# Optimization experiments

Measured on AMD Instinct MI355X. Metric: run time of the kernel, lower is better.

## Reference

```python
import jax, jax.numpy as jnp
import numpy as np

C = 32          # d_model / channels
D_STATE = 32
D_CONV = 4
EXPAND = 2
D_INNER = EXPAND * C          # 64
DT_RANK = (C + 15) // 16      # ceil(32/16) = 2
EPS = 1e-5


def _conv2d(x, w, b):
    # x: (B,C,H,W), w: (O,I,3,3), stride 1, padding 1 (torch Conv2d)
    y = jax.lax.conv_general_dilated(
        x, w, window_strides=(1, 1), padding=[(1, 1), (1, 1)],
        dimension_numbers=("NCHW", "OIHW", "NCHW"))
    return y + b[None, :, None, None]


def _silu(x):
    return x * jax.nn.sigmoid(x)


def _mamba(xs, in_proj_w, conv1d_w, conv1d_b, x_proj_w, dt_proj_w, dt_proj_b,
           A_log, Dp, out_proj_w):
    # xs: (B, L, C)
    xz = xs @ in_proj_w.T                       # (B, L, 2*D_INNER)
    xm, z = jnp.split(xz, 2, axis=-1)           # each (B, L, D_INNER)

    # causal depthwise conv1d along L (torch: padding=d_conv-1 then [..., :L])
    xc = xm.transpose(0, 2, 1)                  # (B, D_INNER, L)
    xc = jax.lax.conv_general_dilated(
        xc, conv1d_w, window_strides=(1,), padding=[(D_CONV - 1, 0)],
        dimension_numbers=("NCH", "OIH", "NCH"),
        feature_group_count=D_INNER)
    xm = _silu((xc + conv1d_b[None, :, None]).transpose(0, 2, 1))  # (B,L,D_INNER)

    x_dbl = xm @ x_proj_w.T                     # (B, L, DT_RANK + 2*D_STATE)
    dt = x_dbl[..., :DT_RANK]
    Bm = x_dbl[..., DT_RANK:DT_RANK + D_STATE]  # (B, L, N)
    Cm = x_dbl[..., DT_RANK + D_STATE:]         # (B, L, N)

    delta = jax.nn.softplus(dt @ dt_proj_w.T + dt_proj_b)  # (B, L, D_INNER)
    A = -jnp.exp(A_log)                                     # (D_INNER, N)

    deltaA = jnp.exp(delta[..., None] * A)                           # (B,L,D,N)
    deltaBx = delta[..., None] * Bm[:, :, None, :] * xm[..., None]   # (B,L,D,N)

    def combine(c1, c2):
        a1, b1 = c1
        a2, b2 = c2
        return a1 * a2, a2 * b1 + b2

    # parallel linear recurrence h_t = deltaA_t * h_{t-1} + deltaBx_t
    _, hstate = jax.lax.associative_scan(combine, (deltaA, deltaBx), axis=1)

    y = jnp.einsum("bldn,bln->bld", hstate, Cm) + xm * Dp
    y = y * _silu(z)
    return y @ out_proj_w.T                     # (B, L, C)


def setup_inputs() -> dict:
    key = jax.random.key(0)
    ks = jax.random.split(key, 16)
    s = 0.02
    inp = {
        "x": jax.random.normal(ks[0], (4, C, 64, 64), dtype=jnp.float32),
        "conv1_w": jax.random.normal(ks[1], (2 * C, C, 3, 3), jnp.float32) * s,
        "conv1_b": jnp.zeros((2 * C,), jnp.float32),
        "conv2_w": jax.random.normal(ks[2], (C, 2 * C, 3, 3), jnp.float32) * s,
        "conv2_b": jnp.zeros((C,), jnp.float32),
        "ln_g": jnp.ones((C,), jnp.float32),
        "ln_b": jnp.zeros((C,), jnp.float32),
        "in_proj_w": jax.random.normal(ks[3], (2 * D_INNER, C), jnp.float32) * s,
        "conv1d_w": jax.random.normal(ks[4], (D_INNER, 1, D_CONV), jnp.float32) * 0.1,
        "conv1d_b": jnp.zeros((D_INNER,), jnp.float32),
        "x_proj_w": jax.random.normal(ks[5], (DT_RANK + 2 * D_STATE, D_INNER), jnp.float32) * s,
        "dt_proj_w": jax.random.normal(ks[6], (D_INNER, DT_RANK), jnp.float32) * 0.1,
        "dt_proj_b": jax.random.normal(ks[7], (D_INNER,), jnp.float32) * 0.1 - 4.0,
        "A_log": jnp.log(jnp.tile(jnp.arange(1, D_STATE + 1, dtype=jnp.float32), (D_INNER, 1))),
        "Dp": jnp.ones((D_INNER,), jnp.float32),
        "out_proj_w": jax.random.normal(ks[8], (C, D_INNER), jnp.float32) * s,
        "smooth_w": jax.random.normal(ks[9], (C, C, 3, 3), jnp.float32) * s,
        "smooth_b": jnp.zeros((C,), jnp.float32),
    }
    return inp


def reference(x, conv1_w, conv1_b, conv2_w, conv2_b, ln_g, ln_b,
              in_proj_w, conv1d_w, conv1d_b, x_proj_w, dt_proj_w, dt_proj_b,
              A_log, Dp, out_proj_w, smooth_w, smooth_b):
    b, c, h, w = x.shape
    # convb residual
    t = jax.nn.relu(_conv2d(x, conv1_w, conv1_b))
    x = _conv2d(t, conv2_w, conv2_b) + x
    # reshape (b,c,h,w) -> (b, h*w, c) row-major (faithful to torch .reshape)
    xs = x.reshape(b, -1, c)
    # LayerNorm over last dim
    mu = jnp.mean(xs, axis=-1, keepdims=True)
    var = jnp.mean(jnp.square(xs - mu), axis=-1, keepdims=True)
    xs = (xs - mu) * jax.lax.rsqrt(var + EPS) * ln_g + ln_b
    # Mamba block
    y = _mamba(xs, in_proj_w, conv1d_w, conv1d_b, x_proj_w, dt_proj_w,
               dt_proj_b, A_log, Dp, out_proj_w)
    y = y.transpose(0, 2, 1).reshape(b, c, h, w)
    return _conv2d(y, smooth_w, smooth_b)
```

## Files before the change

kernel.cpp:

```cpp
#include <hip/hip_runtime.h>
#include <math.h>

#define SEQL 4096
#define L2E 1.44269504088896340736f

#if defined(__has_builtin)
#if __has_builtin(__builtin_amdgcn_exp2f)
#define FAST_EXP2(x) __builtin_amdgcn_exp2f(x)
#endif
#endif
#ifndef FAST_EXP2
#define FAST_EXP2(x) exp2f(x)
#endif

__device__ __forceinline__ float sigmoid_f(float x){ return 1.0f/(1.0f+expf(-x)); }

template<int CI, int CO, int COG, bool RELU, bool RES>
__global__ __launch_bounds__(256) void conv3x3_k(const float* __restrict__ in,
    const float* __restrict__ wgt, const float* __restrict__ bias,
    const float* __restrict__ res, float* __restrict__ out)
{
  constexpr int CIT = CI/4;
  __shared__ float tin[4][2][6][72];
  __shared__ float red[3][4][COG][66];
  const int tid  = threadIdx.x;
  const int lane = tid & 63;
  const int ty   = tid >> 6;
  const int h0   = blockIdx.x * 4;
  const int co0  = blockIdx.y * COG;
  const int b    = blockIdx.z;

  if (lane < 24){
    int cl = lane / 12, rem = lane % 12, r = rem >> 1, side = rem & 1;
    tin[ty][cl][r][side ? 68 : 3] = 0.0f;
  }

  float acc[4][COG];
  #pragma unroll
  for (int rr=0;rr<4;++rr)
    #pragma unroll
    for (int u=0;u<COG;++u) acc[rr][u] = 0.0f;

  const int ci0 = ty*CIT;
  for (int cig = ci0; cig < ci0 + CIT; cig += 2){
    #pragma unroll
    for (int k=0;k<3;++k){
      int idx4 = lane + k*64;
      int row  = idx4 >> 4;
      int cl   = row / 6, r = row - cl*6;
      int w4   = (idx4 & 15) << 2;
      int h    = h0 - 1 + r;
      float4 v = make_float4(0.0f,0.0f,0.0f,0.0f);
      if (h >= 0 && h < 64)
        v = *(const float4*)(in + ((size_t)(b*CI+cig+cl)*64 + h)*64 + w4);
      *(float4*)&tin[ty][cl][r][4+w4] = v;
    }
    #pragma unroll
    for (int cl=0; cl<2; ++cl){
      float rv[6][3];
      #pragma unroll
      for (int r=0;r<6;++r)
        #pragma unroll
        for (int c=0;c<3;++c)
          rv[r][c] = tin[ty][cl][r][3+lane+c];
      #pragma unroll
      for (int u=0;u<COG;++u){
        const float* wp = wgt + ((size_t)(co0+u)*CI + cig + cl)*9;
        #pragma unroll
        for (int rr=0;rr<4;++rr)
          #pragma unroll
          for (int j=0;j<3;++j){
            acc[rr][u] = fmaf(rv[rr+j][0], wp[j*3+0], acc[rr][u]);
            acc[rr][u] = fmaf(rv[rr+j][1], wp[j*3+1], acc[rr][u]);
            acc[rr][u] = fmaf(rv[rr+j][2], wp[j*3+2], acc[rr][u]);
          }
      }
    }
  }
  if (ty > 0){
    #pragma unroll
    for (int rr=0;rr<4;++rr)
      #pragma unroll
      for (int u=0;u<COG;++u) red[ty-1][rr][u][lane] = acc[rr][u];
  }
  __syncthreads();
  if (ty == 0){
    #pragma unroll
    for (int rr=0;rr<4;++rr)
      #pragma unroll
      for (int u=0;u<COG;++u){
        float s = acc[rr][u] + red[0][rr][u][lane] + red[1][rr][u][lane]
                + red[2][rr][u][lane] + bias[co0+u];
        size_t ob = ((size_t)(b*CO+co0+u)*64 + h0+rr)*64 + lane;
        if constexpr (RES)  s += res[ob];
        if constexpr (RELU) s = fmaxf(s, 0.0f);
        out[ob] = s;
      }
  }
}

__global__ __launch_bounds__(512) void mamba_in_k(const float* __restrict__ x2,
    const float* __restrict__ g, const float* __restrict__ be,
    const float* __restrict__ Wip, const float* __restrict__ cw,
    const float* __restrict__ cb, const float* __restrict__ Wxp,
    const float* __restrict__ Wdt, const float* __restrict__ bdt,
    float* __restrict__ xm2, float* __restrict__ szb, float* __restrict__ dlt,
    float* __restrict__ Bm, float* __restrict__ Cm)
{
  __shared__ float xn[68][36];
  __shared__ float xm[64][68];
  __shared__ float xt[64][68];
  __shared__ float xd[64][68];
  const int tid = threadIdx.x, lane = tid & 63, ty = tid >> 6;
  const int bi = blockIdx.x >> 6;
  const int l0 = (blockIdx.x & 63) << 6;

  if (ty < 2){
    int t = ty*64 + lane;
    if (t < 67){
      int tok = l0 - 3 + t;
      if (tok >= 0){
        const float* row = x2 + (size_t)bi*131072 + (size_t)tok*32;
        float v[32];
        #pragma unroll
        for (int c=0;c<32;c+=4){
          float4 f = *(const float4*)(row + c);
          v[c]=f.x; v[c+1]=f.y; v[c+2]=f.z; v[c+3]=f.w;
        }
        float p[8];
        #pragma unroll
        for (int j2=0;j2<8;++j2) p[j2]=v[j2];
        #pragma unroll
        for (int i=8;i<32;i+=8){
          #pragma unroll
          for (int j2=0;j2<8;++j2) p[j2]+=v[i+j2];
        }
        float mu = (((p[0]+p[1])+(p[2]+p[3]))+((p[4]+p[5])+(p[6]+p[7]))) * 0.03125f;
        float q[8];
        #pragma unroll
        for (int j2=0;j2<8;++j2){ float dd=v[j2]-mu; q[j2]=dd*dd; }
        #pragma unroll
        for (int i=8;i<32;i+=8){
          #pragma unroll
          for (int j2=0;j2<8;++j2){ float dd=v[i+j2]-mu; q[j2]+=dd*dd; }
        }
        float var = (((q[0]+q[1])+(q[2]+q[3]))+((q[4]+q[5])+(q[6]+q[7]))) * 0.03125f;
        float rstd = 1.0f / sqrtf(var + 1e-5f);
        #pragma unroll
        for (int c=0;c<32;++c) xn[t][c] = (v[c]-mu)*rstd*g[c] + be[c];
      } else {
        #pragma unroll
        for (int c=0;c<32;++c) xn[t][c] = 0.0f;
      }
    }
  }
  __syncthreads();

  const int d0 = ty*8;
  {
    float xvA[32];
    #pragma unroll
    for (int c=0;c<32;c+=4){
      float4 f = *(const float4*)(&xn[lane][c]);
      xvA[c]=f.x; xvA[c+1]=f.y; xvA[c+2]=f.z; xvA[c+3]=f.w;
    }
    #pragma unroll
    for (int jj=0;jj<8;++jj){
      const float* wr = Wip + (d0+jj)*32;
      float a = 0.0f;
      #pragma unroll
      for (int c=0;c<32;++c) a = fmaf(xvA[c], wr[c], a);
      xm[d0+jj][lane] = a;
    }
  }
  if (lane < 3){
    float xvB[32];
    #pragma unroll
    for (int c=0;c<32;c+=4){
      float4 f = *(const float4*)(&xn[64+lane][c]);
      xvB[c]=f.x; xvB[c+1]=f.y; xvB[c+2]=f.z; xvB[c+3]=f.w;
    }
    #pragma unroll
    for (int jj=0;jj<8;++jj){
      const float* wr = Wip + (d0+jj)*32;
      float a = 0.0f;
      #pragma unroll
      for (int c=0;c<32;++c) a = fmaf(xvB[c], wr[c], a);
      xm[d0+jj][64+lane] = a;
    }
  }
  {
    float xvC[32];
    #pragma unroll
    for (int c=0;c<32;c+=4){
      float4 f = *(const float4*)(&xn[lane+3][c]);
      xvC[c]=f.x; xvC[c+1]=f.y; xvC[c+2]=f.z; xvC[c+3]=f.w;
    }
    #pragma unroll
    for (int jj=0;jj<8;++jj){
      const float* wr = Wip + (64+d0+jj)*32;
      float a = 0.0f;
      #pragma unroll
      for (int c=0;c<32;++c) a = fmaf(xvC[c], wr[c], a);
      szb[((size_t)(bi*64+d0+jj))*SEQL + l0 + lane] = a * sigmoid_f(a);
    }
  }
  __syncthreads();

  #pragma unroll
  for (int jj=0;jj<8;++jj){
    int d = d0 + jj;
    float a = xm[d][lane]*cw[d*4] + xm[d][lane+1]*cw[d*4+1]
            + xm[d][lane+2]*cw[d*4+2] + xm[d][lane+3]*cw[d*4+3] + cb[d];
    float s = a * sigmoid_f(a);
    xt[lane][d] = s;
    xm2[((size_t)(bi*64+d))*SEQL + l0 + lane] = s;
  }
  __syncthreads();

  float xv[64];
  #pragma unroll
  for (int c=0;c<64;c+=4){
    float4 f = *(const float4*)(&xt[lane][c]);
    xv[c]=f.x; xv[c+1]=f.y; xv[c+2]=f.z; xv[c+3]=f.w;
  }
  for (int j=ty; j<66; j+=8){
    const float* wr = Wxp + j*64;
    float a = 0.0f;
    #pragma unroll
    for (int c=0;c<64;++c) a = fmaf(xv[c], wr[c], a);
    xd[lane][j] = a;
  }
  __syncthreads();

  float dt0 = xd[lane][0], dt1 = xd[lane][1];
  #pragma unroll
  for (int k=0;k<8;++k){
    int d2 = ty*8 + k;
    float v = dt0*Wdt[d2*2] + dt1*Wdt[d2*2+1] + bdt[d2];
    float sp = fmaxf(v,0.0f) + log1pf(expf(-fabsf(v)));
    dlt[((size_t)(bi*64+d2))*SEQL + l0 + lane] = sp;
  }
  const int which = ty >> 2, gq = ty & 3;
  float* dst = which ? Cm : Bm;
  size_t base = ((size_t)bi*SEQL + l0 + lane)*32 + gq*8;
  const int s0 = 2 + which*32 + gq*8;
  float4 f0, f1;
  f0.x = xd[lane][s0+0]; f0.y = xd[lane][s0+1]; f0.z = xd[lane][s0+2]; f0.w = xd[lane][s0+3];
  f1.x = xd[lane][s0+4]; f1.y = xd[lane][s0+5]; f1.z = xd[lane][s0+6]; f1.w = xd[lane][s0+7];
  *(float4*)(dst + base)     = f0;
  *(float4*)(dst + base + 4) = f1;
}

__global__ __launch_bounds__(256) void scan_p1(const float* __restrict__ dlt,
    const float* __restrict__ xssm, const float* __restrict__ Bm,
    const float* __restrict__ A_log, float* __restrict__ cA, float* __restrict__ cH)
{
  const int tid = threadIdx.x;
  const int n = tid & 31;
  const int chunk = (blockIdx.x & 7)*8 + (tid >> 5);
  const int bd = blockIdx.x >> 3;
  const int b = bd >> 6, d = bd & 63;
  const int l0 = chunk << 6;
  const float Av2 = -expf(A_log[d*32+n]) * L2E;
  const float* del = dlt  + (size_t)bd*SEQL + l0;
  const float* xp  = xssm + (size_t)bd*SEQL + l0;
  const float* Bp  = Bm + ((size_t)b*SEQL + l0)*32 + n;
  float h = 0.0f, aP = 1.0f;
  #pragma unroll 4
  for (int i0=0;i0<64;i0+=4){
    float4 d4 = *(const float4*)(del+i0);
    float4 x4 = *(const float4*)(xp +i0);
    float b0 = Bp[(i0+0)*32], b1 = Bp[(i0+1)*32], b2 = Bp[(i0+2)*32], b3 = Bp[(i0+3)*32];
    float a0 = FAST_EXP2(d4.x*Av2); h = fmaf(a0,h, d4.x*b0*x4.x); aP *= a0;
    float a1 = FAST_EXP2(d4.y*Av2); h = fmaf(a1,h, d4.y*b1*x4.y); aP *= a1;
    float a2 = FAST_EXP2(d4.z*Av2); h = fmaf(a2,h, d4.z*b2*x4.z); aP *= a2;
    float a3 = FAST_EXP2(d4.w*Av2); h = fmaf(a3,h, d4.w*b3*x4.w); aP *= a3;
  }
  int idx = (bd*64+chunk)*32 + n;
  cA[idx] = aP; cH[idx] = h;
}

__global__ __launch_bounds__(128) void scan_comb(const float* __restrict__ cA,
    float* __restrict__ cH)
{
  const int gid = blockIdx.x*128 + threadIdx.x;
  const int n = gid & 31, bd = gid >> 5;
  const size_t base = (size_t)bd*64*32 + n;
  float hrun = 0.0f;
  #pragma unroll 8
  for (int c=0;c<64;++c){
    float ac = cA[base + c*32];
    float hc = cH[base + c*32];
    cH[base + c*32] = hrun;
    hrun = fmaf(ac, hrun, hc);
  }
}

__global__ __launch_bounds__(256) void scan_p2(const float* __restrict__ dlt,
    const float* __restrict__ xssm, const float* __restrict__ Bm,
    const float* __restrict__ Cm, const float* __restrict__ A_log,
    const float* __restrict__ Dp, const float* __restrict__ sz,
    const float* __restrict__ cH, float* __restrict__ yt)
{
  const int tid = threadIdx.x;
  const int n = tid & 31;
  const int chunk = (blockIdx.x & 7)*8 + (tid >> 5);
  const int bd = blockIdx.x >> 3;
  const int b = bd >> 6, d = bd & 63;
  const int l0 = chunk << 6;
  const float Av2 = -expf(A_log[d*32+n]) * L2E;
  const float Dv = Dp[d];
  const float* del = dlt  + (size_t)bd*SEQL + l0;
  const float* xp  = xssm + (size_t)bd*SEQL + l0;
  const float* szp = sz   + (size_t)bd*SEQL + l0;
  const float* Bp  = Bm + ((size_t)b*SEQL + l0)*32 + n;
  const float* Cp  = Cm + ((size_t)b*SEQL + l0)*32 + n;
  float* yp = yt + (size_t)bd*SEQL + l0;
  float h = cH[(bd*64+chunk)*32 + n];
  #pragma unroll 2
  for (int i0=0;i0<64;i0+=4){
    float4 d4 = *(const float4*)(del+i0);
    float4 x4 = *(const float4*)(xp +i0);
    float4 s4 = *(const float4*)(szp+i0);
    float b0 = Bp[(i0+0)*32], b1 = Bp[(i0+1)*32], b2 = Bp[(i0+2)*32], b3 = Bp[(i0+3)*32];
    float c0 = Cp[(i0+0)*32], c1 = Cp[(i0+1)*32], c2 = Cp[(i0+2)*32], c3 = Cp[(i0+3)*32];
    float a0 = FAST_EXP2(d4.x*Av2); h = fmaf(a0,h, d4.x*b0*x4.x);
    float v0 = h*c0;
    float a1 = FAST_EXP2(d4.y*Av2); h = fmaf(a1,h, d4.y*b1*x4.y);
    float v1 = h*c1;
    float a2 = FAST_EXP2(d4.z*Av2); h = fmaf(a2,h, d4.z*b2*x4.z);
    float v2 = h*c2;
    float a3 = FAST_EXP2(d4.w*Av2); h = fmaf(a3,h, d4.w*b3*x4.w);
    float v3 = h*c3;
    v0 += __shfl_xor(v0,16); v0 += __shfl_xor(v0,8); v0 += __shfl_xor(v0,4);
    v0 += __shfl_xor(v0,2);  v0 += __shfl_xor(v0,1);
    v1 += __shfl_xor(v1,16); v1 += __shfl_xor(v1,8); v1 += __shfl_xor(v1,4);
    v1 += __shfl_xor(v1,2);  v1 += __shfl_xor(v1,1);
    v2 += __shfl_xor(v2,16); v2 += __shfl_xor(v2,8); v2 += __shfl_xor(v2,4);
    v2 += __shfl_xor(v2,2);  v2 += __shfl_xor(v2,1);
    v3 += __shfl_xor(v3,16); v3 += __shfl_xor(v3,8); v3 += __shfl_xor(v3,4);
    v3 += __shfl_xor(v3,2);  v3 += __shfl_xor(v3,1);
    if (n==0){
      yp[i0+0] = fmaf(x4.x, Dv, v0) * s4.x;
      yp[i0+1] = fmaf(x4.y, Dv, v1) * s4.y;
      yp[i0+2] = fmaf(x4.z, Dv, v2) * s4.z;
      yp[i0+3] = fmaf(x4.w, Dv, v3) * s4.w;
    }
  }
}

__global__ __launch_bounds__(512) void outproj_k(const float* __restrict__ yt,
    const float* __restrict__ Wout, float* __restrict__ ym)
{
  __shared__ float ys[64][68];
  const int tid = threadIdx.x, lane = tid & 63, ty = tid >> 6;
  const int bi = blockIdx.x >> 6;
  const int l0 = (blockIdx.x & 63) << 6;
  for (int r=ty; r<64; r+=8)
    ys[lane][r] = yt[((size_t)(bi*64+r))*SEQL + l0 + lane];
  __syncthreads();
  float yv[64];
  #pragma unroll
  for (int c=0;c<64;c+=4){
    float4 f = *(const float4*)(&ys[lane][c]);
    yv[c]=f.x; yv[c+1]=f.y; yv[c+2]=f.z; yv[c+3]=f.w;
  }
  #pragma unroll
  for (int jj=0;jj<4;++jj){
    int j = ty*4 + jj;
    const float* wr = Wout + j*64;
    float acc = 0.0f;
    #pragma unroll
    for (int c=0;c<64;++c) acc = fmaf(yv[c], wr[c], acc);
    ym[((size_t)(bi*32+j))*SEQL + l0 + lane] = acc;
  }
}

extern "C" void kernel_launch(void* const* d_in, const int* in_sizes, int n_in,
                              void* d_out, int out_size, void* d_ws, size_t ws_size,
                              hipStream_t stream) {
  const float* x        = (const float*)d_in[0];
  const float* conv1_w  = (const float*)d_in[1];
  const float* conv1_b  = (const float*)d_in[2];
  const float* conv2_w  = (const float*)d_in[3];
  const float* conv2_b  = (const float*)d_in[4];
  const float* ln_g     = (const float*)d_in[5];
  const float* ln_b     = (const float*)d_in[6];
  const float* in_proj_w= (const float*)d_in[7];
  const float* conv1d_w = (const float*)d_in[8];
  const float* conv1d_b = (const float*)d_in[9];
  const float* x_proj_w = (const float*)d_in[10];
  const float* dt_proj_w= (const float*)d_in[11];
  const float* dt_proj_b= (const float*)d_in[12];
  const float* A_log    = (const float*)d_in[13];
  const float* Dp       = (const float*)d_in[14];
  const float* out_proj_w=(const float*)d_in[15];
  const float* smooth_w = (const float*)d_in[16];
  const float* smooth_b = (const float*)d_in[17];
  float* out = (float*)d_out;

  float* ws = (float*)d_ws;
  float* t      = ws;
  float* x2     = t      + 1048576;
  float* xm2    = x2     + 524288;
  float* szb    = xm2    + 1048576;
  float* dlt    = szb    + 1048576;
  float* Bmat   = dlt    + 1048576;
  float* Cmat   = Bmat   + 524288;
  float* yt     = Cmat   + 524288;
  float* ym     = yt     + 1048576;
  float* cA     = t;
  float* cH     = t + 524288;

  conv3x3_k<32,64,4,true ,false><<<dim3(16,16,4), 256, 0, stream>>>(x,  conv1_w, conv1_b, nullptr, t);
  conv3x3_k<64,32,4,false,true ><<<dim3(16,8,4), 256, 0, stream>>>(t,  conv2_w, conv2_b, x,       x2);
  mamba_in_k  <<<256, 512, 0, stream>>>(x2, ln_g, ln_b, in_proj_w, conv1d_w, conv1d_b,
                                        x_proj_w, dt_proj_w, dt_proj_b,
                                        xm2, szb, dlt, Bmat, Cmat);
  scan_p1     <<<2048, 256, 0, stream>>>(dlt, xm2, Bmat, A_log, cA, cH);
  scan_comb   <<<64,   128, 0, stream>>>(cA, cH);
  scan_p2     <<<2048, 256, 0, stream>>>(dlt, xm2, Bmat, Cmat, A_log, Dp, szb, cH, yt);
  outproj_k   <<<256, 512, 0, stream>>>(yt, out_proj_w, ym);
  conv3x3_k<32,32,4,false,false><<<dim3(16,8,4), 256, 0, stream>>>(ym, smooth_w, smooth_b, nullptr, out);
}
```

Before: 223.6 us.

## Double-buffer conv3x3 input tiles and shrink mamba_in/outproj token tiles for more blocks

The conv3x3 kernel now prefetches the next channel pair into registers while computing the current one, using a double-buffered shared tile. mamba_in_k is restructured to handle 32 tokens per block (512 blocks), and outproj_k handles 16 tokens per block (1024 blocks of 256 threads). The aim is to hide global load latency in the convolutions and to fill more CUs in the projection kernels. In exchange, the conv kernel uses more registers and LDS, and the smaller tiles redo more of the per-block setup work.

```diff
diff --git a/kernel.cpp b/kernel.cpp
--- a/kernel.cpp
+++ b/kernel.cpp
@@ -21,7 +21,8 @@
     const float* __restrict__ res, float* __restrict__ out)
 {
   constexpr int CIT = CI/4;
-  __shared__ float tin[4][2][6][72];
+  constexpr int NCH = CIT/2;
+  __shared__ float tin[4][2][2][6][72];
   __shared__ float red[3][4][COG][66];
   const int tid  = threadIdx.x;
   const int lane = tid & 63;
@@ -30,9 +31,9 @@
   const int co0  = blockIdx.y * COG;
   const int b    = blockIdx.z;
 
-  if (lane < 24){
-    int cl = lane / 12, rem = lane % 12, r = rem >> 1, side = rem & 1;
-    tin[ty][cl][r][side ? 68 : 3] = 0.0f;
+  if (lane < 48){
+    int b2 = lane/24, rem = lane%24, cl = rem/12, rem2 = rem%12, r = rem2>>1, side = rem2&1;
+    tin[ty][b2][cl][r][side ? 68 : 3] = 0.0f;
   }
 
   float acc[4][COG];
@@ -42,27 +43,40 @@
     for (int u=0;u<COG;++u) acc[rr][u] = 0.0f;
 
   const int ci0 = ty*CIT;
-  for (int cig = ci0; cig < ci0 + CIT; cig += 2){
+
+  auto ld = [&](int cig, float4* v){
     #pragma unroll
     for (int k=0;k<3;++k){
-      int idx4 = lane + k*64;
+      int idx4 = lane + (k<<6);
       int row  = idx4 >> 4;
-      int cl   = row / 6, r = row - cl*6;
-      int w4   = (idx4 & 15) << 2;
-      int h    = h0 - 1 + r;
-      float4 v = make_float4(0.0f,0.0f,0.0f,0.0f);
-      if (h >= 0 && h < 64)
-        v = *(const float4*)(in + ((size_t)(b*CI+cig+cl)*64 + h)*64 + w4);
-      *(float4*)&tin[ty][cl][r][4+w4] = v;
-    }
-    #pragma unroll
-    for (int cl=0; cl<2; ++cl){
+      int cl = row/6, r = row - cl*6;
+      int w4 = (idx4 & 15) << 2;
+      int h  = h0 - 1 + r;
+      float4 t = make_float4(0.f,0.f,0.f,0.f);
+      if (h>=0 && h<64)
+        t = *(const float4*)(in + ((size_t)(b*CI+cig+cl)*64 + h)*64 + w4);
+      v[k] = t;
+    }
+  };
+  auto st = [&](int buf, const float4* v){
+    #pragma unroll
+    for (int k=0;k<3;++k){
+      int idx4 = lane + (k<<6);
+      int row  = idx4 >> 4;
+      int cl = row/6, r = row - cl*6;
+      int w4 = (idx4 & 15) << 2;
+      *(float4*)&tin[ty][buf][cl][r][4+w4] = v[k];
+    }
+  };
+  auto comp = [&](int buf, int cig){
+    #pragma unroll
+    for (int cl=0;cl<2;++cl){
       float rv[6][3];
       #pragma unroll
       for (int r=0;r<6;++r)
         #pragma unroll
         for (int c=0;c<3;++c)
-          rv[r][c] = tin[ty][cl][r][3+lane+c];
+          rv[r][c] = tin[ty][buf][cl][r][3+lane+c];
       #pragma unroll
       for (int u=0;u<COG;++u){
         const float* wp = wgt + ((size_t)(co0+u)*CI + cig + cl)*9;
@@ -70,13 +84,24 @@
         for (int rr=0;rr<4;++rr)
           #pragma unroll
           for (int j=0;j<3;++j){
-            acc[rr][u] = fmaf(rv[rr+j][0], wp[j*3+0], acc[rr][u]);
-            acc[rr][u] = fmaf(rv[rr+j][1], wp[j*3+1], acc[rr][u]);
-            acc[rr][u] = fmaf(rv[rr+j][2], wp[j*3+2], acc[rr][u]);
+            acc[rr][u] = fmaf(rv[rr+j][0], wp[3*j+0], acc[rr][u]);
+            acc[rr][u] = fmaf(rv[rr+j][1], wp[3*j+1], acc[rr][u]);
+            acc[rr][u] = fmaf(rv[rr+j][2], wp[3*j+2], acc[rr][u]);
           }
       }
     }
-  }
+  };
+
+  float4 v[3];
+  ld(ci0, v);
+  st(0, v);
+  #pragma unroll 2
+  for (int i=0;i<NCH;++i){
+    if (i+1 < NCH) ld(ci0 + (i+1)*2, v);
+    comp(i&1, ci0 + i*2);
+    if (i+1 < NCH) st((i+1)&1, v);
+  }
+
   if (ty > 0){
     #pragma unroll
     for (int rr=0;rr<4;++rr)
@@ -107,149 +132,132 @@
     float* __restrict__ xm2, float* __restrict__ szb, float* __restrict__ dlt,
     float* __restrict__ Bm, float* __restrict__ Cm)
 {
-  __shared__ float xn[68][36];
-  __shared__ float xm[64][68];
-  __shared__ float xt[64][68];
-  __shared__ float xd[64][68];
-  const int tid = threadIdx.x, lane = tid & 63, ty = tid >> 6;
-  const int bi = blockIdx.x >> 6;
-  const int l0 = (blockIdx.x & 63) << 6;
-
-  if (ty < 2){
-    int t = ty*64 + lane;
-    if (t < 67){
-      int tok = l0 - 3 + t;
-      if (tok >= 0){
-        const float* row = x2 + (size_t)bi*131072 + (size_t)tok*32;
-        float v[32];
+  __shared__ float xn[35][37];
+  __shared__ float xm[64][40];
+  __shared__ float xt[32][68];
+  __shared__ float xd[32][68];
+  const int tid = threadIdx.x;
+  const int bi = blockIdx.x >> 7;
+  const int l0 = (blockIdx.x & 127) << 5;
+
+  if (tid < 35){
+    int tok = l0 - 3 + tid;
+    if (tok >= 0){
+      const float* row = x2 + (size_t)bi*131072 + (size_t)tok*32;
+      float v[32];
+      #pragma unroll
+      for (int c=0;c<32;c+=4){
+        float4 f = *(const float4*)(row + c);
+        v[c]=f.x; v[c+1]=f.y; v[c+2]=f.z; v[c+3]=f.w;
+      }
+      float p[8];
+      #pragma unroll
+      for (int j2=0;j2<8;++j2) p[j2]=v[j2];
+      #pragma unroll
+      for (int i=8;i<32;i+=8){
         #pragma unroll
-        for (int c=0;c<32;c+=4){
-          float4 f = *(const float4*)(row + c);
-          v[c]=f.x; v[c+1]=f.y; v[c+2]=f.z; v[c+3]=f.w;
-        }
-        float p[8];
+        for (int j2=0;j2<8;++j2) p[j2]+=v[i+j2];
+      }
+      float mu = (((p[0]+p[1])+(p[2]+p[3]))+((p[4]+p[5])+(p[6]+p[7]))) * 0.03125f;
+      float q[8];
+      #pragma unroll
+      for (int j2=0;j2<8;++j2){ float dd=v[j2]-mu; q[j2]=dd*dd; }
+      #pragma unroll
+      for (int i=8;i<32;i+=8){
         #pragma unroll
-        for (int j2=0;j2<8;++j2) p[j2]=v[j2];
-        #pragma unroll
-        for (int i=8;i<32;i+=8){
-          #pragma unroll
-          for (int j2=0;j2<8;++j2) p[j2]+=v[i+j2];
-        }
-        float mu = (((p[0]+p[1])+(p[2]+p[3]))+((p[4]+p[5])+(p[6]+p[7]))) * 0.03125f;
-        float q[8];
-        #pragma unroll
-        for (int j2=0;j2<8;++j2){ float dd=v[j2]-mu; q[j2]=dd*dd; }
-        #pragma unroll
-        for (int i=8;i<32;i+=8){
-          #pragma unroll
-          for (int j2=0;j2<8;++j2){ float dd=v[i+j2]-mu; q[j2]+=dd*dd; }
-        }
-        float var = (((q[0]+q[1])+(q[2]+q[3]))+((q[4]+q[5])+(q[6]+q[7]))) * 0.03125f;
-        float rstd = 1.0f / sqrtf(var + 1e-5f);
-        #pragma unroll
-        for (int c=0;c<32;++c) xn[t][c] = (v[c]-mu)*rstd*g[c] + be[c];
-      } else {
-        #pragma unroll
-        for (int c=0;c<32;++c) xn[t][c] = 0.0f;
+        for (int j2=0;j2<8;++j2){ float dd=v[i+j2]-mu; q[j2]+=dd*dd; }
       }
-    }
-  }
-  __syncthreads();
-
-  const int d0 = ty*8;
+      float var = (((q[0]+q[1])+(q[2]+q[3]))+((q[4]+q[5])+(q[6]+q[7]))) * 0.03125f;
+      float rstd = 1.0f / sqrtf(var + 1e-5f);
+      #pragma unroll
+      for (int c=0;c<32;++c) xn[tid][c] = (v[c]-mu)*rstd*g[c] + be[c];
+    } else {
+      #pragma unroll
+      for (int c=0;c<32;++c) xn[tid][c] = 0.0f;
+    }
+  }
+  __syncthreads();
+
   {
-    float xvA[32];
-    #pragma unroll
-    for (int c=0;c<32;c+=4){
-      float4 f = *(const float4*)(&xn[lane][c]);
-      xvA[c]=f.x; xvA[c+1]=f.y; xvA[c+2]=f.z; xvA[c+3]=f.w;
-    }
-    #pragma unroll
-    for (int jj=0;jj<8;++jj){
-      const float* wr = Wip + (d0+jj)*32;
+    const int t5 = tid & 31, jg = tid >> 5;
+    float xv[32];
+    #pragma unroll
+    for (int c=0;c<32;++c) xv[c] = xn[t5+3][c];
+    #pragma unroll
+    for (int k=0;k<8;++k){
+      int j = jg*8 + k;
+      const float* wr = Wip + j*32;
       float a = 0.0f;
       #pragma unroll
-      for (int c=0;c<32;++c) a = fmaf(xvA[c], wr[c], a);
-      xm[d0+jj][lane] = a;
-    }
-  }
-  if (lane < 3){
-    float xvB[32];
-    #pragma unroll
-    for (int c=0;c<32;c+=4){
-      float4 f = *(const float4*)(&xn[64+lane][c]);
-      xvB[c]=f.x; xvB[c+1]=f.y; xvB[c+2]=f.z; xvB[c+3]=f.w;
-    }
-    #pragma unroll
-    for (int jj=0;jj<8;++jj){
-      const float* wr = Wip + (d0+jj)*32;
+      for (int c=0;c<32;++c) a = fmaf(xv[c], wr[c], a);
+      if (j < 64) xm[j][t5+3] = a;
+      else        szb[((size_t)(bi*64 + (j-64)))*SEQL + l0 + t5] = a * sigmoid_f(a);
+    }
+  }
+  if (tid < 192){
+    int tok = tid % 3, j = tid / 3;
+    float xv[32];
+    #pragma unroll
+    for (int c=0;c<32;++c) xv[c] = xn[tok][c];
+    const float* wr = Wip + j*32;
+    float a = 0.0f;
+    #pragma unroll
+    for (int c=0;c<32;++c) a = fmaf(xv[c], wr[c], a);
+    xm[j][tok] = a;
+  }
+  __syncthreads();
+
+  {
+    const int d = tid >> 3, t0 = (tid & 7) << 2;
+    const float w0=cw[d*4], w1=cw[d*4+1], w2=cw[d*4+2], w3=cw[d*4+3], bv=cb[d];
+    float r[4];
+    #pragma unroll
+    for (int k=0;k<4;++k){
+      int t = t0 + k;
+      float a = xm[d][t]*w0 + xm[d][t+1]*w1 + xm[d][t+2]*w2 + xm[d][t+3]*w3 + bv;
+      float s = a * sigmoid_f(a);
+      xt[t][d] = s;
+      r[k] = s;
+    }
+    *(float4*)(xm2 + ((size_t)(bi*64+d))*SEQL + l0 + t0) = make_float4(r[0],r[1],r[2],r[3]);
+  }
+  __syncthreads();
+
+  {
+    const int tok = tid & 31, jg = tid >> 5;
+    float xv[64];
+    #pragma unroll
+    for (int c=0;c<64;c+=4){
+      float4 f = *(const float4*)(&xt[tok][c]);
+      xv[c]=f.x; xv[c+1]=f.y; xv[c+2]=f.z; xv[c+3]=f.w;
+    }
+    for (int j = jg; j < 66; j += 16){
+      const float* wr = Wxp + j*64;
       float a = 0.0f;
       #pragma unroll
-      for (int c=0;c<32;++c) a = fmaf(xvB[c], wr[c], a);
-      xm[d0+jj][64+lane] = a;
-    }
-  }
+      for (int c=0;c<64;++c) a = fmaf(xv[c], wr[c], a);
+      xd[tok][j] = a;
+    }
+  }
+  __syncthreads();
+
   {
-    float xvC[32];
-    #pragma unroll
-    for (int c=0;c<32;c+=4){
-      float4 f = *(const float4*)(&xn[lane+3][c]);
-      xvC[c]=f.x; xvC[c+1]=f.y; xvC[c+2]=f.z; xvC[c+3]=f.w;
-    }
-    #pragma unroll
-    for (int jj=0;jj<8;++jj){
-      const float* wr = Wip + (64+d0+jj)*32;
-      float a = 0.0f;
-      #pragma unroll
-      for (int c=0;c<32;++c) a = fmaf(xvC[c], wr[c], a);
-      szb[((size_t)(bi*64+d0+jj))*SEQL + l0 + lane] = a * sigmoid_f(a);
-    }
-  }
-  __syncthreads();
-
-  #pragma unroll
-  for (int jj=0;jj<8;++jj){
-    int d = d0 + jj;
-    float a = xm[d][lane]*cw[d*4] + xm[d][lane+1]*cw[d*4+1]
-            + xm[d][lane+2]*cw[d*4+2] + xm[d][lane+3]*cw[d*4+3] + cb[d];
-    float s = a * sigmoid_f(a);
-    xt[lane][d] = s;
-    xm2[((size_t)(bi*64+d))*SEQL + l0 + lane] = s;
-  }
-  __syncthreads();
-
-  float xv[64];
-  #pragma unroll
-  for (int c=0;c<64;c+=4){
-    float4 f = *(const float4*)(&xt[lane][c]);
-    xv[c]=f.x; xv[c+1]=f.y; xv[c+2]=f.z; xv[c+3]=f.w;
-  }
-  for (int j=ty; j<66; j+=8){
-    const float* wr = Wxp + j*64;
-    float a = 0.0f;
-    #pragma unroll
-    for (int c=0;c<64;++c) a = fmaf(xv[c], wr[c], a);
-    xd[lane][j] = a;
-  }
-  __syncthreads();
-
-  float dt0 = xd[lane][0], dt1 = xd[lane][1];
-  #pragma unroll
-  for (int k=0;k<8;++k){
-    int d2 = ty*8 + k;
-    float v = dt0*Wdt[d2*2] + dt1*Wdt[d2*2+1] + bdt[d2];
-    float sp = fmaxf(v,0.0f) + log1pf(expf(-fabsf(v)));
-    dlt[((size_t)(bi*64+d2))*SEQL + l0 + lane] = sp;
-  }
-  const int which = ty >> 2, gq = ty & 3;
-  float* dst = which ? Cm : Bm;
-  size_t base = ((size_t)bi*SEQL + l0 + lane)*32 + gq*8;
-  const int s0 = 2 + which*32 + gq*8;
-  float4 f0, f1;
-  f0.x = xd[lane][s0+0]; f0.y = xd[lane][s0+1]; f0.z = xd[lane][s0+2]; f0.w = xd[lane][s0+3];
-  f1.x = xd[lane][s0+4]; f1.y = xd[lane][s0+5]; f1.z = xd[lane][s0+6]; f1.w = xd[lane][s0+7];
-  *(float4*)(dst + base)     = f0;
-  *(float4*)(dst + base + 4) = f1;
+    const int tok = tid & 31, gg = tid >> 5;
+    float dt0 = xd[tok][0], dt1 = xd[tok][1];
+    #pragma unroll
+    for (int k=0;k<4;++k){
+      int d2 = gg*4 + k;
+      float v = dt0*Wdt[d2*2] + dt1*Wdt[d2*2+1] + bdt[d2];
+      float sp = fmaxf(v,0.0f) + log1pf(expf(-fabsf(v)));
+      dlt[((size_t)(bi*64+d2))*SEQL + l0 + tok] = sp;
+    }
+    float* dst = (gg < 8) ? Bm : Cm;
+    int n0 = (gg & 7) * 4;
+    int s0 = 2 + ((gg < 8) ? 0 : 32) + n0;
+    float4 f;
+    f.x = xd[tok][s0]; f.y = xd[tok][s0+1]; f.z = xd[tok][s0+2]; f.w = xd[tok][s0+3];
+    *(float4*)(dst + ((size_t)bi*SEQL + l0 + tok)*32 + n0) = f;
+  }
 }
 
 __global__ __launch_bounds__(256) void scan_p1(const float* __restrict__ dlt,
@@ -350,30 +358,34 @@
   }
 }
 
-__global__ __launch_bounds__(512) void outproj_k(const float* __restrict__ yt,
+__global__ __launch_bounds__(256) void outproj_k(const float* __restrict__ yt,
     const float* __restrict__ Wout, float* __restrict__ ym)
 {
-  __shared__ float ys[64][68];
-  const int tid = threadIdx.x, lane = tid & 63, ty = tid >> 6;
-  const int bi = blockIdx.x >> 6;
-  const int l0 = (blockIdx.x & 63) << 6;
-  for (int r=ty; r<64; r+=8)
-    ys[lane][r] = yt[((size_t)(bi*64+r))*SEQL + l0 + lane];
-  __syncthreads();
+  __shared__ float ys[16][68];
+  const int tid = threadIdx.x;
+  const int bi = blockIdx.x >> 8;
+  const int l0 = (blockIdx.x & 255) << 4;
+  {
+    int d = tid >> 2, t0 = (tid & 3) << 2;
+    float4 f = *(const float4*)(yt + ((size_t)(bi*64+d))*SEQL + l0 + t0);
+    ys[t0][d]=f.x; ys[t0+1][d]=f.y; ys[t0+2][d]=f.z; ys[t0+3][d]=f.w;
+  }
+  __syncthreads();
+  const int tok = tid & 15, jg = tid >> 4;
   float yv[64];
   #pragma unroll
   for (int c=0;c<64;c+=4){
-    float4 f = *(const float4*)(&ys[lane][c]);
+    float4 f = *(const float4*)(&ys[tok][c]);
     yv[c]=f.x; yv[c+1]=f.y; yv[c+2]=f.z; yv[c+3]=f.w;
   }
   #pragma unroll
-  for (int jj=0;jj<4;++jj){
-    int j = ty*4 + jj;
+  for (int k=0;k<2;++k){
+    int j = jg*2 + k;
     const float* wr = Wout + j*64;
     float acc = 0.0f;
     #pragma unroll
     for (int c=0;c<64;++c) acc = fmaf(yv[c], wr[c], acc);
-    ym[((size_t)(bi*32+j))*SEQL + l0 + lane] = acc;
+    ym[((size_t)(bi*32+j))*SEQL + l0 + tok] = acc;
   }
 }
 
@@ -415,12 +427,12 @@
 
   conv3x3_k<32,64,4,true ,false><<<dim3(16,16,4), 256, 0, stream>>>(x,  conv1_w, conv1_b, nullptr, t);
   conv3x3_k<64,32,4,false,true ><<<dim3(16,8,4), 256, 0, stream>>>(t,  conv2_w, conv2_b, x,       x2);
-  mamba_in_k  <<<256, 512, 0, stream>>>(x2, ln_g, ln_b, in_proj_w, conv1d_w, conv1d_b,
+  mamba_in_k  <<<512, 512, 0, stream>>>(x2, ln_g, ln_b, in_proj_w, conv1d_w, conv1d_b,
                                         x_proj_w, dt_proj_w, dt_proj_b,
                                         xm2, szb, dlt, Bmat, Cmat);
   scan_p1     <<<2048, 256, 0, stream>>>(dlt, xm2, Bmat, A_log, cA, cH);
   scan_comb   <<<64,   128, 0, stream>>>(cA, cH);
   scan_p2     <<<2048, 256, 0, stream>>>(dlt, xm2, Bmat, Cmat, A_log, Dp, szb, cH, yt);
-  outproj_k   <<<256, 512, 0, stream>>>(yt, out_proj_w, ym);
+  outproj_k   <<<1024, 256, 0, stream>>>(yt, out_proj_w, ym);
   conv3x3_k<32,32,4,false,false><<<dim3(16,8,4), 256, 0, stream>>>(ym, smooth_w, smooth_b, nullptr, out);
 }
```

Measured after the change: 234.1 us. 4.7% more time.
